# Kernel optimization log

Measured on AMD Instinct MI355X. Metric: run time of the kernel, lower is better.

The kernel has to match this reference:

```python
import jax, jax.numpy as jnp
import numpy as np

B = 32768
ARITY = 6
E = 256          # embedding_size
NF = 512         # num_filters
NR = 50000       # num_roles
NV = 50000       # num_values
BN_EPS = 1e-5


def setup_inputs() -> dict:
    key = jax.random.key(0)
    ks = jax.random.split(key, 7)
    bound = (1.0 / E) ** 0.5
    # padding_idx=0 rows zeroed, matching torch Embedding(padding_idx=0)
    emb_roles = jax.random.uniform(ks[0], (NR, E), minval=-bound, maxval=bound).at[0].set(0.0)
    emb_values = jax.random.uniform(ks[1], (NV, E), minval=-bound, maxval=bound).at[2].set(0.0).at[0].set(0.0)
    # truncated_normal(std=0.1) approximated by clipped normal
    conv1_w = jnp.clip(jax.random.normal(ks[2], (NF, 2, E)), -2.0, 2.0) * 0.1
    conv2_w = jnp.clip(jax.random.normal(ks[3], (NF, 5, E)), -2.0, 2.0) * 0.1
    fc_w = jax.random.normal(ks[4], (1, NF)) * (2.0 / (NF + 1)) ** 0.5  # xavier_normal
    x_batch = jax.random.randint(ks[5], (B, 2 * ARITY), 0, NR, dtype=jnp.int32)
    return dict(
        x_batch=x_batch,
        arity=ARITY,
        emb_roles=emb_roles,
        emb_values=emb_values,
        conv1_w=conv1_w,
        conv1_b=jnp.zeros((NF,), jnp.float32),
        bn1_gamma=jnp.ones((NF,), jnp.float32),
        bn1_beta=jnp.zeros((NF,), jnp.float32),
        conv2_w=conv2_w,
        conv2_b=jnp.zeros((NF,), jnp.float32),
        bn2_gamma=jnp.ones((NF,), jnp.float32),
        bn2_beta=jnp.zeros((NF,), jnp.float32),
        fc_w=fc_w,
        fc_b=jnp.zeros((1,), jnp.float32),
    )


def _bn_relu(x, gamma, beta):
    # x: [B, K, F]; BatchNorm2d in training mode: per-(window-call, channel) stats over batch
    m = jnp.mean(x, axis=0, keepdims=True)
    v = jnp.var(x, axis=0, keepdims=True)  # biased, matches torch normalization
    return jax.nn.relu(gamma * (x - m) * jax.lax.rsqrt(v + BN_EPS) + beta)


def _forward(x_batch, arity, emb_roles, emb_values,
             conv1_w, conv1_b, bn1_gamma, bn1_beta,
             conv2_w, conv2_b, bn2_gamma, bn2_beta, fc_w, fc_b):
    roles = x_batch[:, 0::2]   # [B, arity]
    values = x_batch[:, 1::2]  # [B, arity]
    fr = emb_roles[roles[:, :2]]    # [B, 2, E]
    fv = emb_values[values[:, :2]]  # [B, 2, E]

    # conv1 on two (value, role) windows; kernel (2, E) collapses to a contraction over (2, E)
    win1 = jnp.stack([
        jnp.stack([fv[:, 0], fr[:, 0]], axis=1),
        jnp.stack([fv[:, 1], fr[:, 0]], axis=1),
    ], axis=1)  # [B, 2, 2, E]
    out1 = jnp.einsum('bkre,fre->bkf', win1, conv1_w) + conv1_b
    out1 = _bn_relu(out1, bn1_gamma, bn1_beta)  # [B, 2, F]

    if arity > 2:
        K = arity - 2
        kr = emb_roles[roles[:, 2:]]    # [B, K, E]
        kv = emb_values[values[:, 2:]]  # [B, K, E]
        hrt = jnp.stack([fv[:, 0], fr[:, 0], fv[:, 1]], axis=1)  # [B, 3, E]
        win2 = jnp.concatenate([
            jnp.broadcast_to(hrt[:, None], (hrt.shape[0], K, 3, hrt.shape[-1])),
            kr[:, :, None],
            kv[:, :, None],
        ], axis=2)  # [B, K, 5, E]
        out2 = jnp.einsum('bkre,fre->bkf', win2, conv2_w) + conv2_b
        out2 = _bn_relu(out2, bn2_gamma, bn2_beta)  # [B, K, F]
        allw = jnp.concatenate([out1, out2], axis=1)  # [B, 2+K, F]
    else:
        allw = out1

    min_val = jnp.min(allw, axis=1)  # [B, F]
    return min_val @ fc_w.T + fc_b   # [B, 1]


def reference(x_batch, arity, emb_roles, emb_values,
              conv1_w, conv1_b, bn1_gamma, bn1_beta,
              conv2_w, conv2_b, bn2_gamma, bn2_beta, fc_w, fc_b):
    return _forward(x_batch, arity, emb_roles, emb_values,
                    conv1_w, conv1_b, bn1_gamma, bn1_beta,
                    conv2_w, conv2_b, bn2_gamma, bn2_beta, fc_w, fc_b)
```

## Files before the change

kernel.cpp:

```cpp
#include <hip/hip_runtime.h>
#include <hip/hip_bf16.h>


typedef __hip_bfloat16 bf16;
typedef short bf16x8 __attribute__((ext_vector_type(8)));
typedef float f32x4 __attribute__((ext_vector_type(4)));

#define BATCH 32768
#define MODE_STATS 0
#define MODE_MIN1  1
#define MODE_FINAL 2
#define MODE_STORE 3

__device__ __forceinline__ unsigned short f2b(float f) {
    union { float f; unsigned u; } v; v.f = f;
    unsigned r = v.u + 0x7fffu + ((v.u >> 16) & 1u);
    return (unsigned short)(r >> 16);
}

__global__ __launch_bounds__(256)
void cvt_kernel(const float* __restrict__ src, unsigned short* __restrict__ dst, int n4)
{
    int i = blockIdx.x * 256 + threadIdx.x;
    if (i >= n4) return;
    float4 v = ((const float4*)src)[i];
    ushort4 h;
    h.x = f2b(v.x); h.y = f2b(v.y); h.z = f2b(v.z); h.w = f2b(v.w);
    ((ushort4*)dst)[i] = h;
}

template<int KLEN, int KSTR, int KWOFF, int RPB, int MODE, bool HADD, bool CVTA>
__global__ __launch_bounds__(512, 4)
void gemm_kernel(const int* __restrict__ x, const void* __restrict__ embR_,
                 const void* __restrict__ embV_, const bf16* __restrict__ W,
                 float* __restrict__ accum, const float* __restrict__ coef,
                 bf16* __restrict__ min1, bf16* __restrict__ Hbuf,
                 const float* __restrict__ fcw, float* __restrict__ outacc)
{
    constexpr int KOFF = (RPB == 2) ? 0 : 2;
    __shared__ __align__(16) short Ash[128 * 72];
    __shared__ __align__(16) short Bsh[256 * 72];
    constexpr int NB = 128 / RPB;
    __shared__ int xsh[NB * 12];

    const int tid = threadIdx.x;
    const int lin = blockIdx.x;
    const int m_base = ((lin >> 4) * 8 + (lin & 7)) * 128;
    const int n_base = ((lin >> 3) & 1) * 256;
    const int b0 = m_base / RPB;

    for (int i = tid; i < NB * 12; i += 512) xsh[i] = x[b0 * 12 + i];
    __syncthreads();

    const int lane = tid & 63;
    const int wv   = tid >> 6;
    const int wmb  = (wv >> 2) * 64;
    const int wnb  = (wv & 3) * 64;
    const int quad = lane >> 4;
    const int l16  = lane & 15;

    f32x4 acc[4][4];
    #pragma unroll
    for (int i = 0; i < 4; ++i)
        #pragma unroll
        for (int j = 0; j < 4; ++j)
            acc[i][j] = (f32x4){0.f, 0.f, 0.f, 0.f};

    auto pick = [&](int row, int seg, int& idx, int& isRole) {
        if constexpr (RPB == 1) {
            if      (seg == 0) { idx = xsh[row * 12 + 1]; isRole = 0; }
            else if (seg == 1) { idx = xsh[row * 12 + 0]; isRole = 1; }
            else               { idx = xsh[row * 12 + 3]; isRole = 0; }
        } else if constexpr (RPB == 2) {
            int bl = row >> 1, kk = row & 1;
            if (seg == 0) { idx = xsh[bl * 12 + 2 * kk + 1]; isRole = 0; }
            else          { idx = xsh[bl * 12 + 0];          isRole = 1; }
        } else if constexpr (KLEN == 512) {
            int bl = row >> 2, kk = row & 3;
            if (seg == 0) { idx = xsh[bl * 12 + 2 * kk + 4]; isRole = 1; }
            else          { idx = xsh[bl * 12 + 2 * kk + 5]; isRole = 0; }
        } else {
            int bl = row >> 2, kk = row & 3;
            switch (seg) {
                case 0:  idx = xsh[bl * 12 + 1];          isRole = 0; break;
                case 1:  idx = xsh[bl * 12 + 0];          isRole = 1; break;
                case 2:  idx = xsh[bl * 12 + 3];          isRole = 0; break;
                case 3:  idx = xsh[bl * 12 + 2 * kk + 4]; isRole = 1; break;
                default: idx = xsh[bl * 12 + 2 * kk + 5]; isRole = 0; break;
            }
        }
    };

    constexpr int NCH = KLEN / 64;
    for (int ch = 0; ch < NCH; ++ch) {
        const int k0  = ch * 64;
        const int seg = k0 >> 8;

        if constexpr (CVTA) {
            const float* embRf = (const float*)embR_;
            const float* embVf = (const float*)embV_;
            const int so4 = (k0 & 255) >> 2;
            #pragma unroll
            for (int i = 0; i < 4; ++i) {
                int flat = tid + i * 512;
                int row  = flat >> 4;
                int off4 = flat & 15;
                int idx, isRole;
                pick(row, seg, idx, isRole);
                const float* tab = isRole ? embRf : embVf;
                float4 v = ((const float4*)(tab + (size_t)idx * 256))[so4 + off4];
                ushort4 h;
                h.x = f2b(v.x); h.y = f2b(v.y); h.z = f2b(v.z); h.w = f2b(v.w);
                *(ushort4*)&Ash[row * 72 + off4 * 4] = h;
            }
        } else {
            const bf16* embRb = (const bf16*)embR_;
            const bf16* embVb = (const bf16*)embV_;
            const int so8 = (k0 & 255) >> 3;
            #pragma unroll
            for (int i = 0; i < 2; ++i) {
                int flat = tid + i * 512;
                int row  = flat >> 3;
                int off8 = flat & 7;
                int idx, isRole;
                pick(row, seg, idx, isRole);
                const bf16* tab = isRole ? embRb : embVb;
                uint4 v = ((const uint4*)(tab + (size_t)idx * 256))[so8 + off8];
                *(uint4*)&Ash[row * 72 + off8 * 8] = v;
            }
        }
        #pragma unroll
        for (int i = 0; i < 4; ++i) {
            int flat = tid + i * 512;
            int fr   = flat >> 3;
            int off8 = flat & 7;
            uint4 v = ((const uint4*)(W + (size_t)(n_base + fr) * KSTR + KWOFF + k0))[off8];
            *(uint4*)&Bsh[fr * 72 + off8 * 8] = v;
        }
        __syncthreads();

        #pragma unroll
        for (int ks = 0; ks < 64; ks += 32) {
            bf16x8 af[4], bf_[4];
            #pragma unroll
            for (int t = 0; t < 4; ++t)
                af[t]  = *(const bf16x8*)&Ash[(wmb + t * 16 + l16) * 72 + ks + quad * 8];
            #pragma unroll
            for (int t = 0; t < 4; ++t)
                bf_[t] = *(const bf16x8*)&Bsh[(wnb + t * 16 + l16) * 72 + ks + quad * 8];
            #pragma unroll
            for (int i = 0; i < 4; ++i)
                #pragma unroll
                for (int j = 0; j < 4; ++j)
                    acc[i][j] = __builtin_amdgcn_mfma_f32_16x16x32_bf16(
                        af[i], bf_[j], acc[i][j], 0, 0, 0);
        }
        __syncthreads();
    }

    if constexpr (MODE == MODE_STORE) {
        #pragma unroll
        for (int j = 0; j < 4; ++j) {
            int f = n_base + wnb + j * 16 + l16;
            #pragma unroll
            for (int i = 0; i < 4; ++i)
                #pragma unroll
                for (int r = 0; r < 4; ++r) {
                    int m = m_base + wmb + i * 16 + quad * 4 + r;
                    *(unsigned short*)&Hbuf[(size_t)m * 512 + f] = f2b(acc[i][j][r]);
                }
        }
    } else if constexpr (MODE == MODE_STATS) {
        float* red = (float*)Ash;
        for (int i = tid; i < RPB * 512; i += 512) red[i] = 0.f;
        __syncthreads();
        #pragma unroll
        for (int j = 0; j < 4; ++j) {
            int fl = wnb + j * 16 + l16;
            float sr[4] = {0.f,0.f,0.f,0.f}, qr[4] = {0.f,0.f,0.f,0.f};
            #pragma unroll
            for (int i = 0; i < 4; ++i) {
                float h = 0.f;
                if constexpr (HADD) {
                    int b = b0 + (wmb >> 2) + i * 4 + quad;
                    h = __bfloat162float(Hbuf[(size_t)b * 512 + n_base + fl]);
                }
                #pragma unroll
                for (int r = 0; r < 4; ++r) {
                    float v = acc[i][j][r] + h;
                    sr[r] += v; qr[r] += v * v;
                }
            }
            #pragma unroll
            for (int r = 0; r < 4; ++r) {
                int kk = r % RPB;
                atomicAdd(&red[kk * 256 + fl], sr[r]);
                atomicAdd(&red[RPB * 256 + kk * 256 + fl], qr[r]);
            }
        }
        __syncthreads();
        for (int idx = tid; idx < RPB * 256; idx += 512) {
            int kw = KOFF + (idx >> 8);
            int f  = n_base + (idx & 255);
            atomicAdd(&accum[kw * 512 + f], red[idx]);
            atomicAdd(&accum[3072 + kw * 512 + f], red[RPB * 256 + idx]);
        }
    } else if constexpr (MODE == MODE_MIN1) {
        #pragma unroll
        for (int j = 0; j < 4; ++j) {
            int f = n_base + wnb + j * 16 + l16;
            float a0 = coef[f],        c0 = coef[3072 + f];
            float a1 = coef[512 + f],  c1 = coef[3072 + 512 + f];
            #pragma unroll
            for (int i = 0; i < 4; ++i) {
                #pragma unroll
                for (int rp = 0; rp < 2; ++rp) {
                    int m = m_base + wmb + i * 16 + quad * 4 + rp * 2;
                    float v0 = fmaxf(a0 * acc[i][j][rp * 2]     + c0, 0.f);
                    float v1 = fmaxf(a1 * acc[i][j][rp * 2 + 1] + c1, 0.f);
                    *(unsigned short*)&min1[(size_t)(m >> 1) * 512 + f] =
                        f2b(fminf(v0, v1));
                }
            }
        }
    } else {
        float dotp[4] = {0.f, 0.f, 0.f, 0.f};
        #pragma unroll
        for (int j = 0; j < 4; ++j) {
            int f = n_base + wnb + j * 16 + l16;
            float a[4], c[4];
            #pragma unroll
            for (int r = 0; r < 4; ++r) {
                a[r] = coef[(2 + r) * 512 + f];
                c[r] = coef[3072 + (2 + r) * 512 + f];
            }
            float fw = fcw[f];
            #pragma unroll
            for (int i = 0; i < 4; ++i) {
                int b = b0 + (wmb >> 2) + i * 4 + quad;
                float h = 0.f;
                if constexpr (HADD)
                    h = __bfloat162float(Hbuf[(size_t)b * 512 + f]);
                float mv = 1e30f;
                #pragma unroll
                for (int r = 0; r < 4; ++r)
                    mv = fminf(mv, fmaxf(a[r] * (acc[i][j][r] + h) + c[r], 0.f));
                mv = fminf(mv, __bfloat162float(min1[(size_t)b * 512 + f]));
                dotp[i] += mv * fw;
            }
        }
        #pragma unroll
        for (int i = 0; i < 4; ++i) {
            float v = dotp[i];
            #pragma unroll
            for (int s = 8; s >= 1; s >>= 1) v += __shfl_xor(v, s);
            if (l16 == 0) {
                int b = b0 + (wmb >> 2) + i * 4 + quad;
                atomicAdd(&outacc[b], v);
            }
        }
    }
}

__global__ void bncoef_kernel(const float* __restrict__ accum,
                              const float* __restrict__ g1, const float* __restrict__ be1,
                              const float* __restrict__ g2, const float* __restrict__ be2,
                              float* __restrict__ coef)
{
    int id = blockIdx.x * 256 + threadIdx.x;
    if (id >= 3072) return;
    int kw = id >> 9, f = id & 511;
    float mean = accum[id] * (1.f / BATCH);
    float var  = accum[3072 + id] * (1.f / BATCH) - mean * mean;
    float g  = kw < 2 ? g1[f] : g2[f];
    float be = kw < 2 ? be1[f] : be2[f];
    float a  = g * rsqrtf(var + 1e-5f);
    coef[id] = a;
    coef[3072 + id] = be - a * mean;
}

__global__ void finish_kernel(const float* __restrict__ outacc,
                              const float* __restrict__ fcb, float* __restrict__ out)
{
    int b = blockIdx.x * 256 + threadIdx.x;
    if (b < BATCH)
        out[b] = outacc[b] + fcb[0];
}

extern "C" void kernel_launch(void* const* d_in, const int* in_sizes, int n_in,
                              void* d_out, int out_size, void* d_ws, size_t ws_size,
                              hipStream_t stream)
{
    (void)in_sizes; (void)n_in; (void)out_size;
    const int*   x    = (const int*)  d_in[0];
    const float* embR = (const float*)d_in[2];
    const float* embV = (const float*)d_in[3];
    const float* W1   = (const float*)d_in[4];
    const float* g1   = (const float*)d_in[6];
    const float* be1  = (const float*)d_in[7];
    const float* W2   = (const float*)d_in[8];
    const float* g2   = (const float*)d_in[10];
    const float* be2  = (const float*)d_in[11];
    const float* fcw  = (const float*)d_in[12];
    const float* fcb  = (const float*)d_in[13];

    char* wsb = (char*)d_ws;
    float* accum  = (float*)wsb;
    float* coef   = accum + 6144;
    float* outacc = coef + 6144;
    bf16*  Wbf1   = (bf16*)(wsb + 180224);
    bf16*  Wbf2   = (bf16*)(wsb + 704512);
    bf16*  Hbuf   = (bf16*)(wsb + 2015232);
    bf16*  min1   = (bf16*)(wsb + 35569664);
    bf16*  embRb1 = (bf16*)(wsb + 69124096);
    bf16*  embVb1 = (bf16*)(wsb + 94724096);
    bf16*  min3   = (bf16*)(wsb + 2015232);

    const int tier = (ws_size >= 120324096) ? 1
                   : (ws_size >=  69124096) ? 2 : 3;

    hipMemsetAsync(accum, 0, 6144 * sizeof(float), stream);
    hipMemsetAsync(outacc, 0, BATCH * sizeof(float), stream);
    cvt_kernel<<<256, 256, 0, stream>>>(W1, (unsigned short*)Wbf1, 65536);
    cvt_kernel<<<640, 256, 0, stream>>>(W2, (unsigned short*)Wbf2, 163840);

    if (tier == 1) {
        cvt_kernel<<<12500, 256, 0, stream>>>(embR, (unsigned short*)embRb1, 3200000);
        cvt_kernel<<<12500, 256, 0, stream>>>(embV, (unsigned short*)embVb1, 3200000);
        gemm_kernel<768, 1280, 0, 1, MODE_STORE, false, false><<<512, 512, 0, stream>>>(
            x, embRb1, embVb1, Wbf2, nullptr, nullptr, nullptr, Hbuf, nullptr, nullptr);
        gemm_kernel<512, 512, 0, 2, MODE_STATS, false, false><<<1024, 512, 0, stream>>>(
            x, embRb1, embVb1, Wbf1, accum, nullptr, nullptr, nullptr, nullptr, nullptr);
        gemm_kernel<512, 1280, 768, 4, MODE_STATS, true, false><<<2048, 512, 0, stream>>>(
            x, embRb1, embVb1, Wbf2, accum, nullptr, nullptr, Hbuf, nullptr, nullptr);
        bncoef_kernel<<<12, 256, 0, stream>>>(accum, g1, be1, g2, be2, coef);
        gemm_kernel<512, 512, 0, 2, MODE_MIN1, false, false><<<1024, 512, 0, stream>>>(
            x, embRb1, embVb1, Wbf1, nullptr, coef, min1, nullptr, nullptr, nullptr);
        gemm_kernel<512, 1280, 768, 4, MODE_FINAL, true, false><<<2048, 512, 0, stream>>>(
            x, embRb1, embVb1, Wbf2, nullptr, coef, min1, Hbuf, fcw, outacc);
    } else if (tier == 2) {
        gemm_kernel<768, 1280, 0, 1, MODE_STORE, false, true><<<512, 512, 0, stream>>>(
            x, embR, embV, Wbf2, nullptr, nullptr, nullptr, Hbuf, nullptr, nullptr);
        gemm_kernel<512, 512, 0, 2, MODE_STATS, false, true><<<1024, 512, 0, stream>>>(
            x, embR, embV, Wbf1, accum, nullptr, nullptr, nullptr, nullptr, nullptr);
        gemm_kernel<512, 1280, 768, 4, MODE_STATS, true, true><<<2048, 512, 0, stream>>>(
            x, embR, embV, Wbf2, accum, nullptr, nullptr, Hbuf, nullptr, nullptr);
        bncoef_kernel<<<12, 256, 0, stream>>>(accum, g1, be1, g2, be2, coef);
        gemm_kernel<512, 512, 0, 2, MODE_MIN1, false, true><<<1024, 512, 0, stream>>>(
            x, embR, embV, Wbf1, nullptr, coef, min1, nullptr, nullptr, nullptr);
        gemm_kernel<512, 1280, 768, 4, MODE_FINAL, true, true><<<2048, 512, 0, stream>>>(
            x, embR, embV, Wbf2, nullptr, coef, min1, Hbuf, fcw, outacc);
    } else {
        gemm_kernel<512, 512, 0, 2, MODE_STATS, false, true><<<1024, 512, 0, stream>>>(
            x, embR, embV, Wbf1, accum, nullptr, nullptr, nullptr, nullptr, nullptr);
        gemm_kernel<1280, 1280, 0, 4, MODE_STATS, false, true><<<2048, 512, 0, stream>>>(
            x, embR, embV, Wbf2, accum, nullptr, nullptr, nullptr, nullptr, nullptr);
        bncoef_kernel<<<12, 256, 0, stream>>>(accum, g1, be1, g2, be2, coef);
        gemm_kernel<512, 512, 0, 2, MODE_MIN1, false, true><<<1024, 512, 0, stream>>>(
            x, embR, embV, Wbf1, nullptr, coef, min3, nullptr, nullptr, nullptr);
        gemm_kernel<1280, 1280, 0, 4, MODE_FINAL, false, true><<<2048, 512, 0, stream>>>(
            x, embR, embV, Wbf2, nullptr, coef, min3, nullptr, fcw, outacc);
    }
    finish_kernel<<<128, 256, 0, stream>>>(outacc, fcb, (float*)d_out);
}
```

Baseline: 729.2 us.

## Fuse phase-one stats and H-store GEMMs into one launch with nontemporal accesses

The three phase-one GEMM launches (conv1 stats, conv2 stats, and storing the shared head/relation/tail partial H) are merged into a single p1_kernel that dispatches work by block slot. The conv2 stats are now computed with the full 1280-length contraction instead of reusing Hbuf, which drops the dependency on H and lets every block run in one grid. The aim is to cut launch gaps and tail effects and let the different GEMMs overlap. In exchange the conv2 stats path does more MFMA work, and the slot-based dispatch leaves blocks of uneven length. Hbuf and min1 reads and writes also become nontemporal loads and stores to reduce cache pollution.

```diff
diff --git a/kernel.cpp b/kernel.cpp
--- a/kernel.cpp
+++ b/kernel.cpp
@@ -16,6 +16,12 @@
     union { float f; unsigned u; } v; v.f = f;
     unsigned r = v.u + 0x7fffu + ((v.u >> 16) & 1u);
     return (unsigned short)(r >> 16);
+}
+
+__device__ __forceinline__ float ntb2f(const bf16* p) {
+    unsigned short u = __builtin_nontemporal_load((const unsigned short*)p);
+    union { unsigned x; float f; } v; v.x = ((unsigned)u) << 16;
+    return v.f;
 }
 
 __global__ __launch_bounds__(256)
@@ -30,23 +36,18 @@
 }
 
 template<int KLEN, int KSTR, int KWOFF, int RPB, int MODE, bool HADD, bool CVTA>
-__global__ __launch_bounds__(512, 4)
-void gemm_kernel(const int* __restrict__ x, const void* __restrict__ embR_,
-                 const void* __restrict__ embV_, const bf16* __restrict__ W,
-                 float* __restrict__ accum, const float* __restrict__ coef,
-                 bf16* __restrict__ min1, bf16* __restrict__ Hbuf,
-                 const float* __restrict__ fcw, float* __restrict__ outacc)
+__device__ __forceinline__
+void gemm_body(const int* __restrict__ x, const void* __restrict__ embR_,
+               const void* __restrict__ embV_, const bf16* __restrict__ W,
+               float* __restrict__ accum, const float* __restrict__ coef,
+               bf16* __restrict__ min1, bf16* __restrict__ Hbuf,
+               const float* __restrict__ fcw, float* __restrict__ outacc,
+               short* Ash, short* Bsh, int* xsh,
+               const int m_base, const int n_base)
 {
     constexpr int KOFF = (RPB == 2) ? 0 : 2;
-    __shared__ __align__(16) short Ash[128 * 72];
-    __shared__ __align__(16) short Bsh[256 * 72];
     constexpr int NB = 128 / RPB;
-    __shared__ int xsh[NB * 12];
-
     const int tid = threadIdx.x;
-    const int lin = blockIdx.x;
-    const int m_base = ((lin >> 4) * 8 + (lin & 7)) * 128;
-    const int n_base = ((lin >> 3) & 1) * 256;
     const int b0 = m_base / RPB;
 
     for (int i = tid; i < NB * 12; i += 512) xsh[i] = x[b0 * 12 + i];
@@ -167,7 +168,8 @@
                 #pragma unroll
                 for (int r = 0; r < 4; ++r) {
                     int m = m_base + wmb + i * 16 + quad * 4 + r;
-                    *(unsigned short*)&Hbuf[(size_t)m * 512 + f] = f2b(acc[i][j][r]);
+                    __builtin_nontemporal_store(f2b(acc[i][j][r]),
+                        (unsigned short*)&Hbuf[(size_t)m * 512 + f]);
                 }
         }
     } else if constexpr (MODE == MODE_STATS) {
@@ -183,7 +185,7 @@
                 float h = 0.f;
                 if constexpr (HADD) {
                     int b = b0 + (wmb >> 2) + i * 4 + quad;
-                    h = __bfloat162float(Hbuf[(size_t)b * 512 + n_base + fl]);
+                    h = ntb2f(&Hbuf[(size_t)b * 512 + n_base + fl]);
                 }
                 #pragma unroll
                 for (int r = 0; r < 4; ++r) {
@@ -218,8 +220,8 @@
                     int m = m_base + wmb + i * 16 + quad * 4 + rp * 2;
                     float v0 = fmaxf(a0 * acc[i][j][rp * 2]     + c0, 0.f);
                     float v1 = fmaxf(a1 * acc[i][j][rp * 2 + 1] + c1, 0.f);
-                    *(unsigned short*)&min1[(size_t)(m >> 1) * 512 + f] =
-                        f2b(fminf(v0, v1));
+                    __builtin_nontemporal_store(f2b(fminf(v0, v1)),
+                        (unsigned short*)&min1[(size_t)(m >> 1) * 512 + f]);
                 }
             }
         }
@@ -240,12 +242,12 @@
                 int b = b0 + (wmb >> 2) + i * 4 + quad;
                 float h = 0.f;
                 if constexpr (HADD)
-                    h = __bfloat162float(Hbuf[(size_t)b * 512 + f]);
+                    h = ntb2f(&Hbuf[(size_t)b * 512 + f]);
                 float mv = 1e30f;
                 #pragma unroll
                 for (int r = 0; r < 4; ++r)
                     mv = fminf(mv, fmaxf(a[r] * (acc[i][j][r] + h) + c[r], 0.f));
-                mv = fminf(mv, __bfloat162float(min1[(size_t)b * 512 + f]));
+                mv = fminf(mv, ntb2f(&min1[(size_t)b * 512 + f]));
                 dotp[i] += mv * fw;
             }
         }
@@ -259,6 +261,57 @@
                 atomicAdd(&outacc[b], v);
             }
         }
+    }
+}
+
+template<int KLEN, int KSTR, int KWOFF, int RPB, int MODE, bool HADD, bool CVTA>
+__global__ __launch_bounds__(512, 4)
+void gemm_kernel(const int* __restrict__ x, const void* __restrict__ embR_,
+                 const void* __restrict__ embV_, const bf16* __restrict__ W,
+                 float* __restrict__ accum, const float* __restrict__ coef,
+                 bf16* __restrict__ min1, bf16* __restrict__ Hbuf,
+                 const float* __restrict__ fcw, float* __restrict__ outacc)
+{
+    __shared__ __align__(16) short Ash[128 * 72];
+    __shared__ __align__(16) short Bsh[256 * 72];
+    __shared__ int xsh[128 * 12];
+    const int lin = blockIdx.x;
+    const int m_base = ((lin >> 4) * 8 + (lin & 7)) * 128;
+    const int n_base = ((lin >> 3) & 1) * 256;
+    gemm_body<KLEN, KSTR, KWOFF, RPB, MODE, HADD, CVTA>(
+        x, embR_, embV_, W, accum, coef, min1, Hbuf, fcw, outacc,
+        Ash, Bsh, xsh, m_base, n_base);
+}
+
+template<bool CVTA>
+__global__ __launch_bounds__(512, 4)
+void p1_kernel(const int* __restrict__ x, const void* __restrict__ embR_,
+               const void* __restrict__ embV_, const bf16* __restrict__ W1b,
+               const bf16* __restrict__ W2b, float* __restrict__ accum,
+               bf16* __restrict__ Hbuf)
+{
+    __shared__ __align__(16) short Ash[128 * 72];
+    __shared__ __align__(16) short Bsh[256 * 72];
+    __shared__ int xsh[128 * 12];
+    const int gid  = blockIdx.x / 14;
+    const int slot = blockIdx.x % 14;
+    if (slot < 8) {
+        gemm_body<1280, 1280, 0, 4, MODE_STATS, false, CVTA>(
+            x, embR_, embV_, W2b, accum, nullptr, nullptr, nullptr, nullptr,
+            nullptr, Ash, Bsh, xsh,
+            gid * 512 + (slot >> 1) * 128, (slot & 1) * 256);
+    } else if (slot < 12) {
+        const int j = slot - 8;
+        gemm_body<512, 512, 0, 2, MODE_STATS, false, CVTA>(
+            x, embR_, embV_, W1b, accum, nullptr, nullptr, nullptr, nullptr,
+            nullptr, Ash, Bsh, xsh,
+            gid * 256 + (j >> 1) * 128, (j & 1) * 256);
+    } else {
+        const int j = slot - 12;
+        gemm_body<768, 1280, 0, 1, MODE_STORE, false, CVTA>(
+            x, embR_, embV_, W2b, nullptr, nullptr, nullptr, Hbuf, nullptr,
+            nullptr, Ash, Bsh, xsh,
+            gid * 128, j * 256);
     }
 }
 
@@ -327,24 +380,16 @@
     if (tier == 1) {
         cvt_kernel<<<12500, 256, 0, stream>>>(embR, (unsigned short*)embRb1, 3200000);
         cvt_kernel<<<12500, 256, 0, stream>>>(embV, (unsigned short*)embVb1, 3200000);
-        gemm_kernel<768, 1280, 0, 1, MODE_STORE, false, false><<<512, 512, 0, stream>>>(
-            x, embRb1, embVb1, Wbf2, nullptr, nullptr, nullptr, Hbuf, nullptr, nullptr);
-        gemm_kernel<512, 512, 0, 2, MODE_STATS, false, false><<<1024, 512, 0, stream>>>(
-            x, embRb1, embVb1, Wbf1, accum, nullptr, nullptr, nullptr, nullptr, nullptr);
-        gemm_kernel<512, 1280, 768, 4, MODE_STATS, true, false><<<2048, 512, 0, stream>>>(
-            x, embRb1, embVb1, Wbf2, accum, nullptr, nullptr, Hbuf, nullptr, nullptr);
+        p1_kernel<false><<<3584, 512, 0, stream>>>(
+            x, embRb1, embVb1, Wbf1, Wbf2, accum, Hbuf);
         bncoef_kernel<<<12, 256, 0, stream>>>(accum, g1, be1, g2, be2, coef);
         gemm_kernel<512, 512, 0, 2, MODE_MIN1, false, false><<<1024, 512, 0, stream>>>(
             x, embRb1, embVb1, Wbf1, nullptr, coef, min1, nullptr, nullptr, nullptr);
         gemm_kernel<512, 1280, 768, 4, MODE_FINAL, true, false><<<2048, 512, 0, stream>>>(
             x, embRb1, embVb1, Wbf2, nullptr, coef, min1, Hbuf, fcw, outacc);
     } else if (tier == 2) {
-        gemm_kernel<768, 1280, 0, 1, MODE_STORE, false, true><<<512, 512, 0, stream>>>(
-            x, embR, embV, Wbf2, nullptr, nullptr, nullptr, Hbuf, nullptr, nullptr);
-        gemm_kernel<512, 512, 0, 2, MODE_STATS, false, true><<<1024, 512, 0, stream>>>(
-            x, embR, embV, Wbf1, accum, nullptr, nullptr, nullptr, nullptr, nullptr);
-        gemm_kernel<512, 1280, 768, 4, MODE_STATS, true, true><<<2048, 512, 0, stream>>>(
-            x, embR, embV, Wbf2, accum, nullptr, nullptr, Hbuf, nullptr, nullptr);
+        p1_kernel<true><<<3584, 512, 0, stream>>>(
+            x, embR, embV, Wbf1, Wbf2, accum, Hbuf);
         bncoef_kernel<<<12, 256, 0, stream>>>(accum, g1, be1, g2, be2, coef);
         gemm_kernel<512, 512, 0, 2, MODE_MIN1, false, true><<<1024, 512, 0, stream>>>(
             x, embR, embV, Wbf1, nullptr, coef, min1, nullptr, nullptr, nullptr);
```

New measurement: 1.040 ms. 42.6% more time.

## Fuse stats and final GEMM stages into two persistent-tile passes

Applied to the files above, without the earlier changes.

Replaces the five separate GEMM launches with two kernels. passA computes all BatchNorm sum and sum-of-squares statistics per 128-sample group. It recomputes the full conv2 contraction for every extra window instead of reusing a stored shared-part buffer. passB keeps the conv1 window-min in LDS and the shared conv2 head term in packed registers, then fuses BN, ReLU, min and the fc dot product. This drops the global Hbuf and min1 round trips and several launches, at the cost of extra MFMA work in the stats pass and a large LDS footprint that limits occupancy.

```diff
diff --git a/kernel.cpp b/kernel.cpp
--- a/kernel.cpp
+++ b/kernel.cpp
@@ -7,15 +7,16 @@
 typedef float f32x4 __attribute__((ext_vector_type(4)));
 
 #define BATCH 32768
-#define MODE_STATS 0
-#define MODE_MIN1  1
-#define MODE_FINAL 2
-#define MODE_STORE 3
 
 __device__ __forceinline__ unsigned short f2b(float f) {
     union { float f; unsigned u; } v; v.f = f;
     unsigned r = v.u + 0x7fffu + ((v.u >> 16) & 1u);
     return (unsigned short)(r >> 16);
+}
+
+__device__ __forceinline__ float b2f(unsigned short u) {
+    union { unsigned x; float f; } v; v.x = ((unsigned)u) << 16;
+    return v.f;
 }
 
 __global__ __launch_bounds__(256)
@@ -29,29 +30,40 @@
     ((ushort4*)dst)[i] = h;
 }
 
-template<int KLEN, int KSTR, int KWOFF, int RPB, int MODE, bool HADD, bool CVTA>
-__global__ __launch_bounds__(512, 4)
-void gemm_kernel(const int* __restrict__ x, const void* __restrict__ embR_,
-                 const void* __restrict__ embV_, const bf16* __restrict__ W,
-                 float* __restrict__ accum, const float* __restrict__ coef,
-                 bf16* __restrict__ min1, bf16* __restrict__ Hbuf,
-                 const float* __restrict__ fcw, float* __restrict__ outacc)
-{
-    constexpr int KOFF = (RPB == 2) ? 0 : 2;
-    __shared__ __align__(16) short Ash[128 * 72];
-    __shared__ __align__(16) short Bsh[256 * 72];
-    constexpr int NB = 128 / RPB;
-    __shared__ int xsh[NB * 12];
-
-    const int tid = threadIdx.x;
-    const int lin = blockIdx.x;
-    const int m_base = ((lin >> 4) * 8 + (lin & 7)) * 128;
-    const int n_base = ((lin >> 3) & 1) * 256;
-    const int b0 = m_base / RPB;
-
-    for (int i = tid; i < NB * 12; i += 512) xsh[i] = x[b0 * 12 + i];
-    __syncthreads();
-
+template<int PICK>
+__device__ __forceinline__ void pickfn(const int* xsh, int row, int seg,
+                                       int bloc, int tk, int& idx, int& isRole)
+{
+    if constexpr (PICK == 0) {
+        int bl = (row >> 1) + bloc, kk = row & 1;
+        if (seg == 0) { idx = xsh[bl * 12 + 2 * kk + 1]; isRole = 0; }
+        else          { idx = xsh[bl * 12 + 0];          isRole = 1; }
+    } else if constexpr (PICK == 1) {
+        int bl = (row >> 2) + bloc, kk = row & 3;
+        switch (seg) {
+            case 0:  idx = xsh[bl * 12 + 1];          isRole = 0; break;
+            case 1:  idx = xsh[bl * 12 + 0];          isRole = 1; break;
+            case 2:  idx = xsh[bl * 12 + 3];          isRole = 0; break;
+            case 3:  idx = xsh[bl * 12 + 2 * kk + 4]; isRole = 1; break;
+            default: idx = xsh[bl * 12 + 2 * kk + 5]; isRole = 0; break;
+        }
+    } else if constexpr (PICK == 2) {
+        if      (seg == 0) { idx = xsh[row * 12 + 1]; isRole = 0; }
+        else if (seg == 1) { idx = xsh[row * 12 + 0]; isRole = 1; }
+        else               { idx = xsh[row * 12 + 3]; isRole = 0; }
+    } else {
+        if (seg == 0) { idx = xsh[row * 12 + 2 * tk + 4]; isRole = 1; }
+        else          { idx = xsh[row * 12 + 2 * tk + 5]; isRole = 0; }
+    }
+}
+
+template<int KLEN, int KSTR, int KWOFF, int PICK>
+__device__ __forceinline__ void gemm_acc(
+    const bf16* __restrict__ embR, const bf16* __restrict__ embV,
+    const bf16* __restrict__ W, short* Ash, short* Bsh, const int* xsh,
+    int n_base, int bloc, int tk, f32x4 (&acc)[4][4])
+{
+    const int tid  = threadIdx.x;
     const int lane = tid & 63;
     const int wv   = tid >> 6;
     const int wmb  = (wv >> 2) * 64;
@@ -59,75 +71,27 @@
     const int quad = lane >> 4;
     const int l16  = lane & 15;
 
-    f32x4 acc[4][4];
     #pragma unroll
     for (int i = 0; i < 4; ++i)
         #pragma unroll
         for (int j = 0; j < 4; ++j)
             acc[i][j] = (f32x4){0.f, 0.f, 0.f, 0.f};
-
-    auto pick = [&](int row, int seg, int& idx, int& isRole) {
-        if constexpr (RPB == 1) {
-            if      (seg == 0) { idx = xsh[row * 12 + 1]; isRole = 0; }
-            else if (seg == 1) { idx = xsh[row * 12 + 0]; isRole = 1; }
-            else               { idx = xsh[row * 12 + 3]; isRole = 0; }
-        } else if constexpr (RPB == 2) {
-            int bl = row >> 1, kk = row & 1;
-            if (seg == 0) { idx = xsh[bl * 12 + 2 * kk + 1]; isRole = 0; }
-            else          { idx = xsh[bl * 12 + 0];          isRole = 1; }
-        } else if constexpr (KLEN == 512) {
-            int bl = row >> 2, kk = row & 3;
-            if (seg == 0) { idx = xsh[bl * 12 + 2 * kk + 4]; isRole = 1; }
-            else          { idx = xsh[bl * 12 + 2 * kk + 5]; isRole = 0; }
-        } else {
-            int bl = row >> 2, kk = row & 3;
-            switch (seg) {
-                case 0:  idx = xsh[bl * 12 + 1];          isRole = 0; break;
-                case 1:  idx = xsh[bl * 12 + 0];          isRole = 1; break;
-                case 2:  idx = xsh[bl * 12 + 3];          isRole = 0; break;
-                case 3:  idx = xsh[bl * 12 + 2 * kk + 4]; isRole = 1; break;
-                default: idx = xsh[bl * 12 + 2 * kk + 5]; isRole = 0; break;
-            }
-        }
-    };
 
     constexpr int NCH = KLEN / 64;
     for (int ch = 0; ch < NCH; ++ch) {
         const int k0  = ch * 64;
         const int seg = k0 >> 8;
-
-        if constexpr (CVTA) {
-            const float* embRf = (const float*)embR_;
-            const float* embVf = (const float*)embV_;
-            const int so4 = (k0 & 255) >> 2;
-            #pragma unroll
-            for (int i = 0; i < 4; ++i) {
-                int flat = tid + i * 512;
-                int row  = flat >> 4;
-                int off4 = flat & 15;
-                int idx, isRole;
-                pick(row, seg, idx, isRole);
-                const float* tab = isRole ? embRf : embVf;
-                float4 v = ((const float4*)(tab + (size_t)idx * 256))[so4 + off4];
-                ushort4 h;
-                h.x = f2b(v.x); h.y = f2b(v.y); h.z = f2b(v.z); h.w = f2b(v.w);
-                *(ushort4*)&Ash[row * 72 + off4 * 4] = h;
-            }
-        } else {
-            const bf16* embRb = (const bf16*)embR_;
-            const bf16* embVb = (const bf16*)embV_;
-            const int so8 = (k0 & 255) >> 3;
-            #pragma unroll
-            for (int i = 0; i < 2; ++i) {
-                int flat = tid + i * 512;
-                int row  = flat >> 3;
-                int off8 = flat & 7;
-                int idx, isRole;
-                pick(row, seg, idx, isRole);
-                const bf16* tab = isRole ? embRb : embVb;
-                uint4 v = ((const uint4*)(tab + (size_t)idx * 256))[so8 + off8];
-                *(uint4*)&Ash[row * 72 + off8 * 8] = v;
-            }
+        const int so8 = (k0 & 255) >> 3;
+        #pragma unroll
+        for (int i = 0; i < 2; ++i) {
+            int flat = tid + i * 512;
+            int row  = flat >> 3;
+            int off8 = flat & 7;
+            int idx, isRole;
+            pickfn<PICK>(xsh, row, seg, bloc, tk, idx, isRole);
+            const bf16* tab = isRole ? embR : embV;
+            uint4 v = ((const uint4*)(tab + (size_t)idx * 256))[so8 + off8];
+            *(uint4*)&Ash[row * 72 + off8 * 8] = v;
         }
         #pragma unroll
         for (int i = 0; i < 4; ++i) {
@@ -138,7 +102,6 @@
             *(uint4*)&Bsh[fr * 72 + off8 * 8] = v;
         }
         __syncthreads();
-
         #pragma unroll
         for (int ks = 0; ks < 64; ks += 32) {
             bf16x8 af[4], bf_[4];
@@ -157,109 +120,186 @@
         }
         __syncthreads();
     }
-
-    if constexpr (MODE == MODE_STORE) {
+}
+
+__global__ __launch_bounds__(512, 4)
+void passA_kernel(const int* __restrict__ x, const bf16* __restrict__ embR,
+                  const bf16* __restrict__ embV, const bf16* __restrict__ W1b,
+                  const bf16* __restrict__ W2b, float* __restrict__ accum)
+{
+    __shared__ __align__(16) short Ash[128 * 72];
+    __shared__ __align__(16) short Bsh[256 * 72];
+    __shared__ int   xsh[128 * 12];
+    __shared__ float red[2 * 6 * 256];
+
+    const int tid = threadIdx.x;
+    const int lin = blockIdx.x;
+    const int grp = (lin >> 4) * 8 + (lin & 7);
+    const int nt  = (lin >> 3) & 1;
+    const int n_base = nt * 256;
+
+    for (int i = tid; i < 1536; i += 512) xsh[i] = x[grp * 1536 + i];
+    for (int i = tid; i < 3072; i += 512) red[i] = 0.f;
+    __syncthreads();
+
+    const int lane = tid & 63;
+    const int wv   = tid >> 6;
+    const int wnb  = (wv & 3) * 64;
+    const int l16  = lane & 15;
+
+    f32x4 acc[4][4];
+
+    auto stats = [&](int RPB, int KOFF) {
+        #pragma unroll
+        for (int j = 0; j < 4; ++j) {
+            int fl = wnb + j * 16 + l16;
+            #pragma unroll
+            for (int r = 0; r < 4; ++r) {
+                float sr = 0.f, qr = 0.f;
+                #pragma unroll
+                for (int i = 0; i < 4; ++i) {
+                    float v = acc[i][j][r];
+                    sr += v; qr += v * v;
+                }
+                int kw = KOFF + (r & (RPB - 1));
+                atomicAdd(&red[kw * 256 + fl], sr);
+                atomicAdd(&red[1536 + kw * 256 + fl], qr);
+            }
+        }
+    };
+
+    #pragma unroll 1
+    for (int s = 0; s < 2; ++s) {
+        gemm_acc<512, 512, 0, 0>(embR, embV, W1b, Ash, Bsh, xsh, n_base, s * 64, 0, acc);
+        stats(2, 0);
+    }
+    #pragma unroll 1
+    for (int s = 0; s < 4; ++s) {
+        gemm_acc<1280, 1280, 0, 1>(embR, embV, W2b, Ash, Bsh, xsh, n_base, s * 32, 0, acc);
+        stats(4, 2);
+    }
+    __syncthreads();
+    for (int i = tid; i < 1536; i += 512) {
+        int kw = i >> 8, f = n_base + (i & 255);
+        atomicAdd(&accum[kw * 512 + f], red[i]);
+        atomicAdd(&accum[3072 + kw * 512 + f], red[1536 + i]);
+    }
+}
+
+__global__ __launch_bounds__(512, 2)
+void passB_kernel(const int* __restrict__ x, const bf16* __restrict__ embR,
+                  const bf16* __restrict__ embV, const bf16* __restrict__ W1b,
+                  const bf16* __restrict__ W2b, const float* __restrict__ coef,
+                  const float* __restrict__ fcw, float* __restrict__ outacc)
+{
+    __shared__ __align__(16) short Ash[128 * 72];
+    __shared__ __align__(16) short Bsh[256 * 72];
+    __shared__ int xsh[128 * 12];
+    __shared__ unsigned short m1s[128 * 256];
+
+    const int tid = threadIdx.x;
+    const int lin = blockIdx.x;
+    const int grp = (lin >> 4) * 8 + (lin & 7);
+    const int nt  = (lin >> 3) & 1;
+    const int n_base = nt * 256;
+    const int b0  = grp * 128;
+
+    for (int i = tid; i < 1536; i += 512) xsh[i] = x[b0 * 12 + i];
+    __syncthreads();
+
+    const int lane = tid & 63;
+    const int wv   = tid >> 6;
+    const int wmb  = (wv >> 2) * 64;
+    const int wnb  = (wv & 3) * 64;
+    const int quad = lane >> 4;
+    const int l16  = lane & 15;
+
+    f32x4 acc[4][4];
+
+    #pragma unroll 1
+    for (int s = 0; s < 2; ++s) {
+        gemm_acc<512, 512, 0, 0>(embR, embV, W1b, Ash, Bsh, xsh, n_base, s * 64, 0, acc);
+        #pragma unroll
+        for (int j = 0; j < 4; ++j) {
+            int fl = wnb + j * 16 + l16, f = n_base + fl;
+            float a0 = coef[f],       c0 = coef[3072 + f];
+            float a1 = coef[512 + f], c1 = coef[3584 + f];
+            #pragma unroll
+            for (int i = 0; i < 4; ++i)
+                #pragma unroll
+                for (int rp = 0; rp < 2; ++rp) {
+                    int bl = s * 64 + ((wmb + i * 16 + quad * 4 + rp * 2) >> 1);
+                    float v0 = fmaxf(a0 * acc[i][j][rp * 2]     + c0, 0.f);
+                    float v1 = fmaxf(a1 * acc[i][j][rp * 2 + 1] + c1, 0.f);
+                    m1s[bl * 256 + fl] = f2b(fminf(v0, v1));
+                }
+        }
+    }
+
+    gemm_acc<768, 1280, 0, 2>(embR, embV, W2b, Ash, Bsh, xsh, n_base, 0, 0, acc);
+    unsigned hpk[4][4][2];
+    #pragma unroll
+    for (int i = 0; i < 4; ++i)
+        #pragma unroll
+        for (int j = 0; j < 4; ++j) {
+            hpk[i][j][0] = (unsigned)f2b(acc[i][j][0]) | ((unsigned)f2b(acc[i][j][1]) << 16);
+            hpk[i][j][1] = (unsigned)f2b(acc[i][j][2]) | ((unsigned)f2b(acc[i][j][3]) << 16);
+        }
+
+    f32x4 m2[4][4];
+    #pragma unroll
+    for (int i = 0; i < 4; ++i)
+        #pragma unroll
+        for (int j = 0; j < 4; ++j)
+            m2[i][j] = (f32x4){1e30f, 1e30f, 1e30f, 1e30f};
+    #pragma unroll 1
+    for (int tk = 0; tk < 4; ++tk) {
+        gemm_acc<512, 1280, 768, 3>(embR, embV, W2b, Ash, Bsh, xsh, n_base, 0, tk, acc);
         #pragma unroll
         for (int j = 0; j < 4; ++j) {
             int f = n_base + wnb + j * 16 + l16;
+            float a = coef[(2 + tk) * 512 + f];
+            float c = coef[3072 + (2 + tk) * 512 + f];
             #pragma unroll
             for (int i = 0; i < 4; ++i)
                 #pragma unroll
                 for (int r = 0; r < 4; ++r) {
-                    int m = m_base + wmb + i * 16 + quad * 4 + r;
-                    *(unsigned short*)&Hbuf[(size_t)m * 512 + f] = f2b(acc[i][j][r]);
+                    unsigned u = hpk[i][j][r >> 1];
+                    float h = b2f((unsigned short)((r & 1) ? (u >> 16) : (u & 0xffffu)));
+                    float v = fmaxf(a * (acc[i][j][r] + h) + c, 0.f);
+                    m2[i][j][r] = fminf(m2[i][j][r], v);
                 }
         }
-    } else if constexpr (MODE == MODE_STATS) {
-        float* red = (float*)Ash;
-        for (int i = tid; i < RPB * 512; i += 512) red[i] = 0.f;
-        __syncthreads();
-        #pragma unroll
-        for (int j = 0; j < 4; ++j) {
-            int fl = wnb + j * 16 + l16;
-            float sr[4] = {0.f,0.f,0.f,0.f}, qr[4] = {0.f,0.f,0.f,0.f};
-            #pragma unroll
-            for (int i = 0; i < 4; ++i) {
-                float h = 0.f;
-                if constexpr (HADD) {
-                    int b = b0 + (wmb >> 2) + i * 4 + quad;
-                    h = __bfloat162float(Hbuf[(size_t)b * 512 + n_base + fl]);
-                }
-                #pragma unroll
-                for (int r = 0; r < 4; ++r) {
-                    float v = acc[i][j][r] + h;
-                    sr[r] += v; qr[r] += v * v;
-                }
+    }
+
+    float dotv[4][4];
+    #pragma unroll
+    for (int i = 0; i < 4; ++i)
+        #pragma unroll
+        for (int r = 0; r < 4; ++r) dotv[i][r] = 0.f;
+    #pragma unroll
+    for (int j = 0; j < 4; ++j) {
+        int fl = wnb + j * 16 + l16;
+        float fw = fcw[n_base + fl];
+        #pragma unroll
+        for (int i = 0; i < 4; ++i)
+            #pragma unroll
+            for (int r = 0; r < 4; ++r) {
+                int bl = wmb + i * 16 + quad * 4 + r;
+                float m1v = b2f(m1s[bl * 256 + fl]);
+                dotv[i][r] += fminf(m1v, m2[i][j][r]) * fw;
             }
-            #pragma unroll
-            for (int r = 0; r < 4; ++r) {
-                int kk = r % RPB;
-                atomicAdd(&red[kk * 256 + fl], sr[r]);
-                atomicAdd(&red[RPB * 256 + kk * 256 + fl], qr[r]);
-            }
-        }
-        __syncthreads();
-        for (int idx = tid; idx < RPB * 256; idx += 512) {
-            int kw = KOFF + (idx >> 8);
-            int f  = n_base + (idx & 255);
-            atomicAdd(&accum[kw * 512 + f], red[idx]);
-            atomicAdd(&accum[3072 + kw * 512 + f], red[RPB * 256 + idx]);
-        }
-    } else if constexpr (MODE == MODE_MIN1) {
-        #pragma unroll
-        for (int j = 0; j < 4; ++j) {
-            int f = n_base + wnb + j * 16 + l16;
-            float a0 = coef[f],        c0 = coef[3072 + f];
-            float a1 = coef[512 + f],  c1 = coef[3072 + 512 + f];
-            #pragma unroll
-            for (int i = 0; i < 4; ++i) {
-                #pragma unroll
-                for (int rp = 0; rp < 2; ++rp) {
-                    int m = m_base + wmb + i * 16 + quad * 4 + rp * 2;
-                    float v0 = fmaxf(a0 * acc[i][j][rp * 2]     + c0, 0.f);
-                    float v1 = fmaxf(a1 * acc[i][j][rp * 2 + 1] + c1, 0.f);
-                    *(unsigned short*)&min1[(size_t)(m >> 1) * 512 + f] =
-                        f2b(fminf(v0, v1));
-                }
-            }
-        }
-    } else {
-        float dotp[4] = {0.f, 0.f, 0.f, 0.f};
-        #pragma unroll
-        for (int j = 0; j < 4; ++j) {
-            int f = n_base + wnb + j * 16 + l16;
-            float a[4], c[4];
-            #pragma unroll
-            for (int r = 0; r < 4; ++r) {
-                a[r] = coef[(2 + r) * 512 + f];
-                c[r] = coef[3072 + (2 + r) * 512 + f];
-            }
-            float fw = fcw[f];
-            #pragma unroll
-            for (int i = 0; i < 4; ++i) {
-                int b = b0 + (wmb >> 2) + i * 4 + quad;
-                float h = 0.f;
-                if constexpr (HADD)
-                    h = __bfloat162float(Hbuf[(size_t)b * 512 + f]);
-                float mv = 1e30f;
-                #pragma unroll
-                for (int r = 0; r < 4; ++r)
-                    mv = fminf(mv, fmaxf(a[r] * (acc[i][j][r] + h) + c[r], 0.f));
-                mv = fminf(mv, __bfloat162float(min1[(size_t)b * 512 + f]));
-                dotp[i] += mv * fw;
-            }
-        }
-        #pragma unroll
-        for (int i = 0; i < 4; ++i) {
-            float v = dotp[i];
-            #pragma unroll
-            for (int s = 8; s >= 1; s >>= 1) v += __shfl_xor(v, s);
-            if (l16 == 0) {
-                int b = b0 + (wmb >> 2) + i * 4 + quad;
-                atomicAdd(&outacc[b], v);
-            }
-        }
-    }
+    }
+    #pragma unroll
+    for (int i = 0; i < 4; ++i)
+        #pragma unroll
+        for (int r = 0; r < 4; ++r) {
+            float v = dotv[i][r];
+            v += __shfl_xor(v, 1); v += __shfl_xor(v, 2);
+            v += __shfl_xor(v, 4); v += __shfl_xor(v, 8);
+            if (l16 == 0)
+                atomicAdd(&outacc[b0 + wmb + i * 16 + quad * 4 + r], v);
+        }
 }
 
 __global__ void bncoef_kernel(const float* __restrict__ accum,
@@ -291,7 +331,7 @@
                               void* d_out, int out_size, void* d_ws, size_t ws_size,
                               hipStream_t stream)
 {
-    (void)in_sizes; (void)n_in; (void)out_size;
+    (void)in_sizes; (void)n_in; (void)out_size; (void)ws_size;
     const int*   x    = (const int*)  d_in[0];
     const float* embR = (const float*)d_in[2];
     const float* embV = (const float*)d_in[3];
@@ -310,56 +350,18 @@
     float* outacc = coef + 6144;
     bf16*  Wbf1   = (bf16*)(wsb + 180224);
     bf16*  Wbf2   = (bf16*)(wsb + 704512);
-    bf16*  Hbuf   = (bf16*)(wsb + 2015232);
-    bf16*  min1   = (bf16*)(wsb + 35569664);
-    bf16*  embRb1 = (bf16*)(wsb + 69124096);
-    bf16*  embVb1 = (bf16*)(wsb + 94724096);
-    bf16*  min3   = (bf16*)(wsb + 2015232);
-
-    const int tier = (ws_size >= 120324096) ? 1
-                   : (ws_size >=  69124096) ? 2 : 3;
+    bf16*  embRb  = (bf16*)(wsb + 2015232);
+    bf16*  embVb  = (bf16*)(wsb + 27615232);
 
     hipMemsetAsync(accum, 0, 6144 * sizeof(float), stream);
     hipMemsetAsync(outacc, 0, BATCH * sizeof(float), stream);
     cvt_kernel<<<256, 256, 0, stream>>>(W1, (unsigned short*)Wbf1, 65536);
     cvt_kernel<<<640, 256, 0, stream>>>(W2, (unsigned short*)Wbf2, 163840);
-
-    if (tier == 1) {
-        cvt_kernel<<<12500, 256, 0, stream>>>(embR, (unsigned short*)embRb1, 3200000);
-        cvt_kernel<<<12500, 256, 0, stream>>>(embV, (unsigned short*)embVb1, 3200000);
-        gemm_kernel<768, 1280, 0, 1, MODE_STORE, false, false><<<512, 512, 0, stream>>>(
-            x, embRb1, embVb1, Wbf2, nullptr, nullptr, nullptr, Hbuf, nullptr, nullptr);
-        gemm_kernel<512, 512, 0, 2, MODE_STATS, false, false><<<1024, 512, 0, stream>>>(
-            x, embRb1, embVb1, Wbf1, accum, nullptr, nullptr, nullptr, nullptr, nullptr);
-        gemm_kernel<512, 1280, 768, 4, MODE_STATS, true, false><<<2048, 512, 0, stream>>>(
-            x, embRb1, embVb1, Wbf2, accum, nullptr, nullptr, Hbuf, nullptr, nullptr);
-        bncoef_kernel<<<12, 256, 0, stream>>>(accum, g1, be1, g2, be2, coef);
-        gemm_kernel<512, 512, 0, 2, MODE_MIN1, false, false><<<1024, 512, 0, stream>>>(
-            x, embRb1, embVb1, Wbf1, nullptr, coef, min1, nullptr, nullptr, nullptr);
-        gemm_kernel<512, 1280, 768, 4, MODE_FINAL, true, false><<<2048, 512, 0, stream>>>(
-            x, embRb1, embVb1, Wbf2, nullptr, coef, min1, Hbuf, fcw, outacc);
-    } else if (tier == 2) {
-        gemm_kernel<768, 1280, 0, 1, MODE_STORE, false, true><<<512, 512, 0, stream>>>(
-            x, embR, embV, Wbf2, nullptr, nullptr, nullptr, Hbuf, nullptr, nullptr);
-        gemm_kernel<512, 512, 0, 2, MODE_STATS, false, true><<<1024, 512, 0, stream>>>(
-            x, embR, embV, Wbf1, accum, nullptr, nullptr, nullptr, nullptr, nullptr);
-        gemm_kernel<512, 1280, 768, 4, MODE_STATS, true, true><<<2048, 512, 0, stream>>>(
-            x, embR, embV, Wbf2, accum, nullptr, nullptr, Hbuf, nullptr, nullptr);
-        bncoef_kernel<<<12, 256, 0, stream>>>(accum, g1, be1, g2, be2, coef);
-        gemm_kernel<512, 512, 0, 2, MODE_MIN1, false, true><<<1024, 512, 0, stream>>>(
-            x, embR, embV, Wbf1, nullptr, coef, min1, nullptr, nullptr, nullptr);
-        gemm_kernel<512, 1280, 768, 4, MODE_FINAL, true, true><<<2048, 512, 0, stream>>>(
-            x, embR, embV, Wbf2, nullptr, coef, min1, Hbuf, fcw, outacc);
-    } else {
-        gemm_kernel<512, 512, 0, 2, MODE_STATS, false, true><<<1024, 512, 0, stream>>>(
-            x, embR, embV, Wbf1, accum, nullptr, nullptr, nullptr, nullptr, nullptr);
-        gemm_kernel<1280, 1280, 0, 4, MODE_STATS, false, true><<<2048, 512, 0, stream>>>(
-            x, embR, embV, Wbf2, accum, nullptr, nullptr, nullptr, nullptr, nullptr);
-        bncoef_kernel<<<12, 256, 0, stream>>>(accum, g1, be1, g2, be2, coef);
-        gemm_kernel<512, 512, 0, 2, MODE_MIN1, false, true><<<1024, 512, 0, stream>>>(
-            x, embR, embV, Wbf1, nullptr, coef, min3, nullptr, nullptr, nullptr);
-        gemm_kernel<1280, 1280, 0, 4, MODE_FINAL, false, true><<<2048, 512, 0, stream>>>(
-            x, embR, embV, Wbf2, nullptr, coef, min3, nullptr, fcw, outacc);
-    }
+    cvt_kernel<<<12500, 256, 0, stream>>>(embR, (unsigned short*)embRb, 3200000);
+    cvt_kernel<<<12500, 256, 0, stream>>>(embV, (unsigned short*)embVb, 3200000);
+
+    passA_kernel<<<512, 512, 0, stream>>>(x, embRb, embVb, Wbf1, Wbf2, accum);
+    bncoef_kernel<<<12, 256, 0, stream>>>(accum, g1, be1, g2, be2, coef);
+    passB_kernel<<<512, 512, 0, stream>>>(x, embRb, embVb, Wbf1, Wbf2, coef, fcw, outacc);
     finish_kernel<<<128, 256, 0, stream>>>(outacc, fcb, (float*)d_out);
 }
```

Result: slower. 1.101 ms (+50.9%).

## Double-buffer gathered A tile with register prefetch; read weights directly from global

Applied to the files above, without the earlier changes.

The gathered embedding tile is now loaded into registers one chunk ahead and written into one of two alternating shared-memory buffers, which removes one barrier per chunk and overlaps the gather latency with the MFMA work. The weight operand no longer goes through shared memory: each lane loads its bf16x8 fragments straight from global memory, relying on the cache. This frees LDS and removes staging stores, but adds redundant global weight traffic across the four waves sharing a column block and raises register pressure from the prefetch buffers.

```diff
diff --git a/kernel.cpp b/kernel.cpp
--- a/kernel.cpp
+++ b/kernel.cpp
@@ -38,8 +38,7 @@
                  const float* __restrict__ fcw, float* __restrict__ outacc)
 {
     constexpr int KOFF = (RPB == 2) ? 0 : 2;
-    __shared__ __align__(16) short Ash[128 * 72];
-    __shared__ __align__(16) short Bsh[256 * 72];
+    __shared__ __align__(16) short Ash[2 * 128 * 72];
     constexpr int NB = 128 / RPB;
     __shared__ int xsh[NB * 12];
 
@@ -91,11 +90,12 @@
         }
     };
 
-    constexpr int NCH = KLEN / 64;
-    for (int ch = 0; ch < NCH; ++ch) {
+    float4 pf[4];
+    uint4  pu[2];
+
+    auto issueA = [&](int ch) {
         const int k0  = ch * 64;
         const int seg = k0 >> 8;
-
         if constexpr (CVTA) {
             const float* embRf = (const float*)embR_;
             const float* embVf = (const float*)embV_;
@@ -108,10 +108,7 @@
                 int idx, isRole;
                 pick(row, seg, idx, isRole);
                 const float* tab = isRole ? embRf : embVf;
-                float4 v = ((const float4*)(tab + (size_t)idx * 256))[so4 + off4];
-                ushort4 h;
-                h.x = f2b(v.x); h.y = f2b(v.y); h.z = f2b(v.z); h.w = f2b(v.w);
-                *(ushort4*)&Ash[row * 72 + off4 * 4] = h;
+                pf[i] = ((const float4*)(tab + (size_t)idx * 256))[so4 + off4];
             }
         } else {
             const bf16* embRb = (const bf16*)embR_;
@@ -125,29 +122,54 @@
                 int idx, isRole;
                 pick(row, seg, idx, isRole);
                 const bf16* tab = isRole ? embRb : embVb;
-                uint4 v = ((const uint4*)(tab + (size_t)idx * 256))[so8 + off8];
-                *(uint4*)&Ash[row * 72 + off8 * 8] = v;
-            }
-        }
-        #pragma unroll
-        for (int i = 0; i < 4; ++i) {
-            int flat = tid + i * 512;
-            int fr   = flat >> 3;
-            int off8 = flat & 7;
-            uint4 v = ((const uint4*)(W + (size_t)(n_base + fr) * KSTR + KWOFF + k0))[off8];
-            *(uint4*)&Bsh[fr * 72 + off8 * 8] = v;
-        }
+                pu[i] = ((const uint4*)(tab + (size_t)idx * 256))[so8 + off8];
+            }
+        }
+    };
+    auto writeA = [&](short* As) {
+        if constexpr (CVTA) {
+            #pragma unroll
+            for (int i = 0; i < 4; ++i) {
+                int flat = tid + i * 512;
+                int row  = flat >> 4;
+                int off4 = flat & 15;
+                ushort4 h;
+                h.x = f2b(pf[i].x); h.y = f2b(pf[i].y);
+                h.z = f2b(pf[i].z); h.w = f2b(pf[i].w);
+                *(ushort4*)&As[row * 72 + off4 * 4] = h;
+            }
+        } else {
+            #pragma unroll
+            for (int i = 0; i < 2; ++i) {
+                int flat = tid + i * 512;
+                int row  = flat >> 3;
+                int off8 = flat & 7;
+                *(uint4*)&As[row * 72 + off8 * 8] = pu[i];
+            }
+        }
+    };
+
+    const bf16* wlane = W + (size_t)(n_base + wnb + l16) * KSTR + KWOFF + quad * 8;
+
+    constexpr int NCH = KLEN / 64;
+    issueA(0);
+    int buf = 0;
+    #pragma unroll 1
+    for (int ch = 0; ch < NCH; ++ch) {
+        short* As = Ash + buf * (128 * 72);
+        writeA(As);
+        if (ch + 1 < NCH) issueA(ch + 1);
         __syncthreads();
-
+        const int k0 = ch * 64;
         #pragma unroll
         for (int ks = 0; ks < 64; ks += 32) {
             bf16x8 af[4], bf_[4];
             #pragma unroll
             for (int t = 0; t < 4; ++t)
-                af[t]  = *(const bf16x8*)&Ash[(wmb + t * 16 + l16) * 72 + ks + quad * 8];
+                af[t]  = *(const bf16x8*)&As[(wmb + t * 16 + l16) * 72 + ks + quad * 8];
             #pragma unroll
             for (int t = 0; t < 4; ++t)
-                bf_[t] = *(const bf16x8*)&Bsh[(wnb + t * 16 + l16) * 72 + ks + quad * 8];
+                bf_[t] = *(const bf16x8*)(wlane + (size_t)t * 16 * KSTR + k0 + ks);
             #pragma unroll
             for (int i = 0; i < 4; ++i)
                 #pragma unroll
@@ -155,8 +177,9 @@
                     acc[i][j] = __builtin_amdgcn_mfma_f32_16x16x32_bf16(
                         af[i], bf_[j], acc[i][j], 0, 0, 0);
         }
-        __syncthreads();
+        buf ^= 1;
     }
+    __syncthreads();
 
     if constexpr (MODE == MODE_STORE) {
         #pragma unroll
```

New measurement: 1.030 ms. +41.2%, slower.
